# Kernel optimization log

Hardware: AMD Instinct MI355X
Metric: run time of the kernel (lower is better)

Reference implementation:

```python
import jax, jax.numpy as jnp
import numpy as np


def _conv1x1(X, W, b):
    # X: [B,C,H,W], W: [Cout,Cin], b: [Cout] -> [B,Cout,H,W]
    return jnp.einsum('oc,bchw->bohw', W, X) + b[None, :, None, None]


def setup_inputs() -> dict:
    key = jax.random.key(0)
    ks = jax.random.split(key, 7)
    B, C, H, W = 8, 512, 32, 32
    scale = 1.0 / np.sqrt(C)
    return {
        'X': jax.random.normal(ks[0], (B, C, H, W), dtype=jnp.float32),
        'W_phi': jax.random.normal(ks[1], (C, C), dtype=jnp.float32) * scale,
        'b_phi': jnp.zeros((C,), dtype=jnp.float32),
        'W_theta': jax.random.normal(ks[2], (C, C), dtype=jnp.float32) * scale,
        'b_theta': jnp.zeros((C,), dtype=jnp.float32),
        'W_beta': jax.random.normal(ks[3], (C, C), dtype=jnp.float32) * scale,
        'b_beta': jnp.zeros((C,), dtype=jnp.float32),
    }


def reference(X, W_phi, b_phi, W_theta, b_theta, W_beta, b_beta):
    B, C, H, W = X.shape
    N = H * W
    phi = _conv1x1(X, W_phi, b_phi).reshape(B, -1, N)      # [B,Co,N]
    theta = _conv1x1(X, W_theta, b_theta).reshape(B, -1, N)  # [B,Co,N]
    beta = _conv1x1(X, W_beta, b_beta).reshape(B, -1, N)    # [B,Co,N]
    # attention over spatial positions: scores [B,N,N], row-softmax
    A = jax.nn.softmax(jnp.einsum('bcn,bcm->bnm', phi, theta), axis=-1)
    Z = jnp.einsum('bcn,bnm->bcm', beta, A)                 # [B,Co,N]
    return Z.reshape(B, -1, H, W) + X
```

## Files before the change

### kernel.cpp

```cpp
#include <hip/hip_runtime.h>

typedef __bf16 bf16_t;
typedef __bf16 bf16x4 __attribute__((ext_vector_type(4)));
typedef __bf16 bf16x8 __attribute__((ext_vector_type(8)));
typedef _Float16 f16_t;
typedef _Float16 f16x4 __attribute__((ext_vector_type(4)));
typedef _Float16 f16x8 __attribute__((ext_vector_type(8)));
typedef float  f32x4  __attribute__((ext_vector_type(4)));

#define BK 64
#define BATCH 8
#define CDIM 512
#define NSP 1024
#define SOFF 90.0f

__device__ __forceinline__ void gl2lds16(const void* g, void* l) {
    __builtin_amdgcn_global_load_lds(
        (const __attribute__((address_space(1))) void*)g,
        (__attribute__((address_space(3))) void*)l, 16, 0, 0);
}

template<typename T, int NW>
__device__ __forceinline__ void stage128x64(const T* __restrict__ src, int ld, T* dst) {
    int lane = threadIdx.x & 63;
    int wave = threadIdx.x >> 6;
    constexpr int SPW = 16 / NW;
    int colsw = ((lane & 7) ^ (lane >> 3)) << 3;
#pragma unroll
    for (int c = 0; c < SPW; ++c) {
        int seg = wave * SPW + c;
        int row = (seg << 3) + (lane >> 3);
        const T* g = src + (size_t)row * ld + colsw;
        T* l = dst + (seg << 9);
        gl2lds16(g, l);
    }
}

__device__ __forceinline__ f32x4 mfma_op(f16x8 a, f16x8 b, f32x4 c) {
    return __builtin_amdgcn_mfma_f32_16x16x32_f16(a, b, c, 0, 0, 0);
}
__device__ __forceinline__ f32x4 mfma_op(bf16x8 a, bf16x8 b, f32x4 c) {
    return __builtin_amdgcn_mfma_f32_16x16x32_bf16(a, b, c, 0, 0, 0);
}

template<typename VT, typename T, int NW, int MI, int NI>
__device__ __forceinline__ void gemm_core(const T* __restrict__ A, int lda,
                                          const T* __restrict__ B, int ldb, int K,
                                          T* sA, T* sB, f32x4 acc[MI][NI]) {
    int lane = threadIdx.x & 63;
    int wave = threadIdx.x >> 6;
    int wr = (wave >> 1) * (MI * 16);
    int wc = (wave & 1) * (NI * 16);
    int fr = lane & 15;
    int q  = lane >> 4;

    for (int k0 = 0; k0 < K; k0 += BK) {
        stage128x64<T, NW>(A + k0, lda, sA);
        stage128x64<T, NW>(B + k0, ldb, sB);
        __syncthreads();
#pragma unroll
        for (int kk = 0; kk < 2; ++kk) {
            int sc = ((((kk << 2) + q) ^ (fr & 7)) << 3);
            VT a[MI], b[NI];
#pragma unroll
            for (int i = 0; i < MI; ++i)
                a[i] = *reinterpret_cast<const VT*>(sA + (wr + i*16 + fr)*BK + sc);
#pragma unroll
            for (int j = 0; j < NI; ++j)
                b[j] = *reinterpret_cast<const VT*>(sB + (wc + j*16 + fr)*BK + sc);
#pragma unroll
            for (int mi = 0; mi < MI; ++mi)
#pragma unroll
                for (int ni = 0; ni < NI; ++ni)
                    acc[mi][ni] = mfma_op(a[mi], b[ni], acc[mi][ni]);
        }
        __syncthreads();
    }
}

__global__ __launch_bounds__(256)
void prep_kernel(const float* __restrict__ X, const float* __restrict__ Wp,
                 const float* __restrict__ Wt, const float* __restrict__ Wb,
                 f16_t* __restrict__ Xt, f16_t* __restrict__ W16) {
    int z = blockIdx.z;
    int tx = threadIdx.x;
    int ty = threadIdx.y;
    if (z == 8) {
        int g = (blockIdx.y * 32 + blockIdx.x) * 256 + ty * 8 + tx;
        if (g < 98304) {
            int i = g << 3;
            int r = i >> 9, c = i & 511;
            const float* src = (r < 512) ? (Wp + ((size_t)r << 9))
                             : (r < 1024) ? (Wt + ((size_t)(r - 512) << 9))
                                          : (Wb + ((size_t)(r - 1024) << 9));
            float4 v0 = *reinterpret_cast<const float4*>(src + c);
            float4 v1 = *reinterpret_cast<const float4*>(src + c + 4);
            f16x8 o;
            o[0]=(f16_t)v0.x; o[1]=(f16_t)v0.y; o[2]=(f16_t)v0.z; o[3]=(f16_t)v0.w;
            o[4]=(f16_t)v1.x; o[5]=(f16_t)v1.y; o[6]=(f16_t)v1.z; o[7]=(f16_t)v1.w;
            *reinterpret_cast<f16x8*>(W16 + i) = o;
        }
        return;
    }
    __shared__ float tile[32][33];
    const float* x = X + (size_t)z * CDIM * NSP;
    int c0 = blockIdx.y * 32, n0 = blockIdx.x * 32;
    float4 v = *reinterpret_cast<const float4*>(x + (size_t)(c0 + ty) * NSP + n0 + tx * 4);
    tile[ty][tx * 4 + 0] = v.x;
    tile[ty][tx * 4 + 1] = v.y;
    tile[ty][tx * 4 + 2] = v.z;
    tile[ty][tx * 4 + 3] = v.w;
    __syncthreads();
    f16x4 o;
#pragma unroll
    for (int i = 0; i < 4; ++i) o[i] = (f16_t)tile[tx * 4 + i][ty];
    *reinterpret_cast<f16x4*>(Xt + (size_t)z * NSP * CDIM + (size_t)(n0 + ty) * CDIM + c0 + tx * 4) = o;
}

__global__ __launch_bounds__(256, 4)
void conv_kernel(const f16_t* __restrict__ Xt, const f16_t* __restrict__ W16,
                 const float* __restrict__ bias_phi, const float* __restrict__ bias_theta,
                 const float* __restrict__ bias_beta,
                 f16_t* __restrict__ phiH, f16_t* __restrict__ thH,
                 bf16_t* __restrict__ betaB) {
    __shared__ alignas(16) f16_t sA[128 * BK], sB[128 * BK];
    int b = blockIdx.z;
    int n0 = blockIdx.y * 128;
    int col0 = blockIdx.x * 128;
    const f16_t* A = Xt + ((size_t)b * NSP + n0) * CDIM;
    const f16_t* B = W16 + (size_t)col0 * CDIM;
    f32x4 acc[4][4];
#pragma unroll
    for (int i = 0; i < 4; i++)
#pragma unroll
        for (int j = 0; j < 4; j++)
#pragma unroll
            for (int e = 0; e < 4; e++) acc[i][j][e] = 0.0f;
    gemm_core<f16x8, f16_t, 4, 4, 4>(A, CDIM, B, CDIM, CDIM, sA, sB, acc);

    int lane = threadIdx.x & 63;
    int wave = threadIdx.x >> 6;
    int wr = (wave >> 1) << 6, wc = (wave & 1) << 6;
    int fr = lane & 15, q4 = ((lane >> 4) << 2);

    if (col0 < 1024) {
        bool isPhi = (col0 < 512);
        const float* bias = isPhi ? bias_phi : bias_theta;
        f16_t* dh = (isPhi ? phiH : thH) + (size_t)b * NSP * CDIM;
        int oc0 = col0 & 511;
#pragma unroll
        for (int mi = 0; mi < 4; mi++)
#pragma unroll
            for (int ni = 0; ni < 4; ni++) {
                int col = oc0 + wc + ni * 16 + fr;
                float bv = bias[col];
#pragma unroll
                for (int e = 0; e < 4; e++) {
                    int row = n0 + wr + mi * 16 + q4 + e;
                    dh[(size_t)row * CDIM + col] = (f16_t)(acc[mi][ni][e] + bv);
                }
            }
    } else {
        bf16_t* dst = betaB + (size_t)b * CDIM * NSP;
#pragma unroll
        for (int mi = 0; mi < 4; mi++)
#pragma unroll
            for (int ni = 0; ni < 4; ni++) {
                int c = (col0 - 1024) + wc + ni * 16 + fr;
                float bv = bias_beta[c];
                int rowb = n0 + wr + mi * 16 + q4;
                bf16x4 v;
#pragma unroll
                for (int e = 0; e < 4; e++) v[e] = (bf16_t)(acc[mi][ni][e] + bv);
                *reinterpret_cast<bf16x4*>(dst + (size_t)c * NSP + rowb) = v;
            }
    }
}

__global__ __launch_bounds__(256, 4)
void sgemm_kernel(const f16_t* __restrict__ phiH, const f16_t* __restrict__ thH,
                  bf16_t* __restrict__ Et, float* __restrict__ psum) {
    __shared__ alignas(16) f16_t sA[128 * BK], sB[128 * BK];
    int b = blockIdx.z;
    int n0 = blockIdx.y * 128;
    int m0 = blockIdx.x * 128;
    const f16_t* A = phiH + ((size_t)b * NSP + n0) * CDIM;
    const f16_t* B = thH + ((size_t)b * NSP + m0) * CDIM;
    f32x4 acc[4][4];
#pragma unroll
    for (int i = 0; i < 4; i++)
#pragma unroll
        for (int j = 0; j < 4; j++)
#pragma unroll
            for (int e = 0; e < 4; e++) acc[i][j][e] = 0.0f;
    gemm_core<f16x8, f16_t, 4, 4, 4>(A, CDIM, B, CDIM, CDIM, sA, sB, acc);

    bf16_t* et = Et + (size_t)b * NSP * NSP;
    int lane = threadIdx.x & 63;
    int wave = threadIdx.x >> 6;
    int wr = (wave >> 1) << 6, wc = (wave & 1) << 6;
    int fr = lane & 15, q4 = ((lane >> 4) << 2);

    float p[4][4];
#pragma unroll
    for (int mi = 0; mi < 4; mi++)
#pragma unroll
        for (int e = 0; e < 4; e++) p[mi][e] = 0.0f;

#pragma unroll
    for (int mi = 0; mi < 4; mi++)
#pragma unroll
        for (int ni = 0; ni < 4; ni++) {
            int col = m0 + wc + ni * 16 + fr;
            int rowb = n0 + wr + mi * 16 + q4;
            bf16x4 v;
#pragma unroll
            for (int e = 0; e < 4; e++) {
                float ev = __expf(acc[mi][ni][e] - SOFF);
                p[mi][e] += ev;
                v[e] = (bf16_t)ev;
            }
            *reinterpret_cast<bf16x4*>(et + (size_t)col * NSP + rowb) = v;
        }

#pragma unroll
    for (int mi = 0; mi < 4; mi++)
#pragma unroll
        for (int e = 0; e < 4; e++) {
#pragma unroll
            for (int off = 1; off < 16; off <<= 1)
                p[mi][e] += __shfl_xor(p[mi][e], off);
        }
    if ((lane & 15) == 0) {
        int pidx = blockIdx.x * 2 + (wc >> 6);
        float* ps = psum + ((size_t)b * 16 + pidx) * NSP;
#pragma unroll
        for (int mi = 0; mi < 4; mi++)
#pragma unroll
            for (int e = 0; e < 4; e++)
                ps[n0 + wr + mi * 16 + q4 + e] = p[mi][e];
    }
}

__global__ __launch_bounds__(256)
void norm_kernel(const float* __restrict__ psum, const bf16_t* __restrict__ betaB,
                 bf16_t* __restrict__ beta2) {
    __shared__ float rs[NSP];
    int b  = blockIdx.x >> 4;
    int cc = (blockIdx.x & 15) << 5;
    int tid = threadIdx.x;
#pragma unroll
    for (int i = 0; i < 4; ++i) {
        int n = i * 256 + tid;
        float s = 0.f;
#pragma unroll
        for (int pp = 0; pp < 16; ++pp) s += psum[((size_t)b * 16 + pp) * NSP + n];
        rs[n] = 1.0f / s;
    }
    __syncthreads();
#pragma unroll
    for (int it = 0; it < 16; ++it) {
        int row = cc + it * 2 + (tid >> 7);
        int n = (tid & 127) << 3;
        size_t base = ((size_t)b * CDIM + row) * NSP + n;
        bf16x8 v = *reinterpret_cast<const bf16x8*>(betaB + base);
        bf16x8 o;
#pragma unroll
        for (int e = 0; e < 8; ++e) o[e] = (bf16_t)((float)v[e] * rs[n + e]);
        *reinterpret_cast<bf16x8*>(beta2 + base) = o;
    }
}

__global__ __launch_bounds__(512, 2)
void zgemm_kernel(const bf16_t* __restrict__ beta2, const bf16_t* __restrict__ Et,
                  const float* __restrict__ X, float* __restrict__ out) {
    __shared__ alignas(16) bf16_t sA[128 * BK], sB[128 * BK];
    int b = blockIdx.z;
    int c0 = blockIdx.y * 128;
    int m0 = blockIdx.x * 128;
    const bf16_t* A = beta2 + ((size_t)b * CDIM + c0) * NSP;
    const bf16_t* B = Et + ((size_t)b * NSP + m0) * NSP;
    f32x4 acc[2][4];
#pragma unroll
    for (int i = 0; i < 2; i++)
#pragma unroll
        for (int j = 0; j < 4; j++)
#pragma unroll
            for (int e = 0; e < 4; e++) acc[i][j][e] = 0.0f;
    gemm_core<bf16x8, bf16_t, 8, 2, 4>(A, NSP, B, NSP, NSP, sA, sB, acc);

    const float* xs = X + (size_t)b * CDIM * NSP;
    float* dst = out + (size_t)b * CDIM * NSP;
    int lane = threadIdx.x & 63;
    int wave = threadIdx.x >> 6;
    int wr = (wave >> 1) << 5, wc = (wave & 1) << 6;
    int fr = lane & 15, q4 = ((lane >> 4) << 2);
#pragma unroll
    for (int mi = 0; mi < 2; mi++)
#pragma unroll
        for (int ni = 0; ni < 4; ni++) {
            int col = m0 + wc + ni * 16 + fr;
#pragma unroll
            for (int e = 0; e < 4; e++) {
                int row = c0 + wr + mi * 16 + q4 + e;
                size_t idx = (size_t)row * NSP + col;
                dst[idx] = acc[mi][ni][e] + xs[idx];
            }
        }
}

extern "C" void kernel_launch(void* const* d_in, const int* in_sizes, int n_in,
                              void* d_out, int out_size, void* d_ws, size_t ws_size,
                              hipStream_t stream) {
    const float* X  = (const float*)d_in[0];
    const float* Wp = (const float*)d_in[1];
    const float* bp = (const float*)d_in[2];
    const float* Wt = (const float*)d_in[3];
    const float* bt = (const float*)d_in[4];
    const float* Wb = (const float*)d_in[5];
    const float* bb = (const float*)d_in[6];
    float* out = (float*)d_out;

    char* ws = (char*)d_ws;
    size_t off = 0;
    auto alloc = [&](size_t bytes) -> char* {
        char* p = ws + off;
        off += (bytes + 255) & ~(size_t)255;
        return p;
    };

    const size_t BNC2 = (size_t)BATCH * NSP * CDIM * 2;
    f16_t*  Xt16  = (f16_t*)alloc(BNC2);
    f16_t*  W16   = (f16_t*)alloc((size_t)1536 * 512 * 2);
    f16_t*  phiH  = (f16_t*)alloc(BNC2);
    f16_t*  thH   = (f16_t*)alloc(BNC2);
    bf16_t* betaB = (bf16_t*)alloc(BNC2);
    bf16_t* beta2 = (bf16_t*)alloc(BNC2);
    bf16_t* Et    = (bf16_t*)alloc((size_t)BATCH * NSP * NSP * 2);
    float*  psum  = (float*)alloc((size_t)BATCH * 16 * NSP * 4);

    prep_kernel<<<dim3(32, 16, 9), dim3(8, 32), 0, stream>>>(X, Wp, Wt, Wb, Xt16, W16);
    conv_kernel<<<dim3(12, 8, BATCH), dim3(256), 0, stream>>>(Xt16, W16, bp, bt, bb,
                                                              phiH, thH, betaB);
    sgemm_kernel<<<dim3(8, 8, BATCH), dim3(256), 0, stream>>>(phiH, thH, Et, psum);
    norm_kernel<<<dim3(128), dim3(256), 0, stream>>>(psum, betaB, beta2);
    zgemm_kernel<<<dim3(8, 4, BATCH), dim3(512), 0, stream>>>(beta2, Et, X, out);

    (void)in_sizes; (void)n_in; (void)out_size; (void)ws_size;
}
```

Baseline: 79.11 us.

## Fuse softmax normalization into Z GEMM and co-schedule beta conv with scores

The beta 1x1 conv is moved out of the phi/theta conv launch and runs as extra blocks of the score GEMM kernel, so the two independent workloads share one launch. The separate norm kernel goes away: the Z GEMM reduces the softmax row sums into LDS itself and scales the beta tile by the reciprocals while staging it into LDS. The Z GEMM tile also shrinks to 64x128 with 2x2 MFMA tiles per wave, giving more blocks. This removes one launch and one full write and read of the scaled beta buffer. In exchange, every Z block recomputes the 1024 reciprocal sums, and the A tile is staged through registers instead of direct global-to-LDS loads.

```diff
diff --git a/kernel.cpp b/kernel.cpp
--- a/kernel.cpp
+++ b/kernel.cpp
@@ -31,8 +31,7 @@
         int seg = wave * SPW + c;
         int row = (seg << 3) + (lane >> 3);
         const T* g = src + (size_t)row * ld + colsw;
-        T* l = dst + (seg << 9);
-        gl2lds16(g, l);
+        gl2lds16(g, dst + (seg << 9));
     }
 }
 
@@ -43,39 +42,48 @@
     return __builtin_amdgcn_mfma_f32_16x16x32_bf16(a, b, c, 0, 0, 0);
 }
 
-template<typename VT, typename T, int NW, int MI, int NI>
-__device__ __forceinline__ void gemm_core(const T* __restrict__ A, int lda,
-                                          const T* __restrict__ B, int ldb, int K,
-                                          T* sA, T* sB, f32x4 acc[MI][NI]) {
+template<typename VT, typename T>
+__device__ __forceinline__ void gemm128_4w(const T* __restrict__ A, int lda,
+                                           const T* __restrict__ B, int ldb, int K,
+                                           T* sA, T* sB, f32x4 acc[4][4]) {
     int lane = threadIdx.x & 63;
     int wave = threadIdx.x >> 6;
-    int wr = (wave >> 1) * (MI * 16);
-    int wc = (wave & 1) * (NI * 16);
+    int wr = (wave >> 1) << 6;
+    int wc = (wave & 1) << 6;
     int fr = lane & 15;
     int q  = lane >> 4;
 
     for (int k0 = 0; k0 < K; k0 += BK) {
-        stage128x64<T, NW>(A + k0, lda, sA);
-        stage128x64<T, NW>(B + k0, ldb, sB);
+        stage128x64<T, 4>(A + k0, lda, sA);
+        stage128x64<T, 4>(B + k0, ldb, sB);
         __syncthreads();
 #pragma unroll
         for (int kk = 0; kk < 2; ++kk) {
             int sc = ((((kk << 2) + q) ^ (fr & 7)) << 3);
-            VT a[MI], b[NI];
-#pragma unroll
-            for (int i = 0; i < MI; ++i)
+            VT a[4], b[4];
+#pragma unroll
+            for (int i = 0; i < 4; ++i)
                 a[i] = *reinterpret_cast<const VT*>(sA + (wr + i*16 + fr)*BK + sc);
 #pragma unroll
-            for (int j = 0; j < NI; ++j)
+            for (int j = 0; j < 4; ++j)
                 b[j] = *reinterpret_cast<const VT*>(sB + (wc + j*16 + fr)*BK + sc);
 #pragma unroll
-            for (int mi = 0; mi < MI; ++mi)
-#pragma unroll
-                for (int ni = 0; ni < NI; ++ni)
+            for (int mi = 0; mi < 4; ++mi)
+#pragma unroll
+                for (int ni = 0; ni < 4; ++ni)
                     acc[mi][ni] = mfma_op(a[mi], b[ni], acc[mi][ni]);
         }
         __syncthreads();
     }
+}
+
+__device__ __forceinline__ void zero44(f32x4 acc[4][4]) {
+#pragma unroll
+    for (int i = 0; i < 4; i++)
+#pragma unroll
+        for (int j = 0; j < 4; j++)
+#pragma unroll
+            for (int e = 0; e < 4; e++) acc[i][j][e] = 0.0f;
 }
 
 __global__ __launch_bounds__(256)
@@ -118,187 +126,203 @@
 }
 
 __global__ __launch_bounds__(256, 4)
-void conv_kernel(const f16_t* __restrict__ Xt, const f16_t* __restrict__ W16,
-                 const float* __restrict__ bias_phi, const float* __restrict__ bias_theta,
-                 const float* __restrict__ bias_beta,
-                 f16_t* __restrict__ phiH, f16_t* __restrict__ thH,
-                 bf16_t* __restrict__ betaB) {
+void conv_pt_kernel(const f16_t* __restrict__ Xt, const f16_t* __restrict__ W16,
+                    const float* __restrict__ bias_phi, const float* __restrict__ bias_theta,
+                    f16_t* __restrict__ phiH, f16_t* __restrict__ thH) {
     __shared__ alignas(16) f16_t sA[128 * BK], sB[128 * BK];
     int b = blockIdx.z;
     int n0 = blockIdx.y * 128;
     int col0 = blockIdx.x * 128;
-    const f16_t* A = Xt + ((size_t)b * NSP + n0) * CDIM;
-    const f16_t* B = W16 + (size_t)col0 * CDIM;
     f32x4 acc[4][4];
-#pragma unroll
-    for (int i = 0; i < 4; i++)
-#pragma unroll
-        for (int j = 0; j < 4; j++)
-#pragma unroll
-            for (int e = 0; e < 4; e++) acc[i][j][e] = 0.0f;
-    gemm_core<f16x8, f16_t, 4, 4, 4>(A, CDIM, B, CDIM, CDIM, sA, sB, acc);
+    zero44(acc);
+    gemm128_4w<f16x8, f16_t>(Xt + ((size_t)b * NSP + n0) * CDIM, CDIM,
+                             W16 + (size_t)col0 * CDIM, CDIM, CDIM, sA, sB, acc);
 
     int lane = threadIdx.x & 63;
     int wave = threadIdx.x >> 6;
     int wr = (wave >> 1) << 6, wc = (wave & 1) << 6;
     int fr = lane & 15, q4 = ((lane >> 4) << 2);
 
-    if (col0 < 1024) {
-        bool isPhi = (col0 < 512);
-        const float* bias = isPhi ? bias_phi : bias_theta;
-        f16_t* dh = (isPhi ? phiH : thH) + (size_t)b * NSP * CDIM;
-        int oc0 = col0 & 511;
-#pragma unroll
-        for (int mi = 0; mi < 4; mi++)
-#pragma unroll
-            for (int ni = 0; ni < 4; ni++) {
-                int col = oc0 + wc + ni * 16 + fr;
-                float bv = bias[col];
-#pragma unroll
-                for (int e = 0; e < 4; e++) {
-                    int row = n0 + wr + mi * 16 + q4 + e;
-                    dh[(size_t)row * CDIM + col] = (f16_t)(acc[mi][ni][e] + bv);
-                }
-            }
-    } else {
-        bf16_t* dst = betaB + (size_t)b * CDIM * NSP;
-#pragma unroll
-        for (int mi = 0; mi < 4; mi++)
-#pragma unroll
-            for (int ni = 0; ni < 4; ni++) {
-                int c = (col0 - 1024) + wc + ni * 16 + fr;
-                float bv = bias_beta[c];
-                int rowb = n0 + wr + mi * 16 + q4;
-                bf16x4 v;
-#pragma unroll
-                for (int e = 0; e < 4; e++) v[e] = (bf16_t)(acc[mi][ni][e] + bv);
-                *reinterpret_cast<bf16x4*>(dst + (size_t)c * NSP + rowb) = v;
-            }
-    }
+    bool isPhi = (col0 < 512);
+    const float* bias = isPhi ? bias_phi : bias_theta;
+    f16_t* dh = (isPhi ? phiH : thH) + (size_t)b * NSP * CDIM;
+    int oc0 = col0 & 511;
+#pragma unroll
+    for (int mi = 0; mi < 4; mi++)
+#pragma unroll
+        for (int ni = 0; ni < 4; ni++) {
+            int col = oc0 + wc + ni * 16 + fr;
+            float bv = bias[col];
+#pragma unroll
+            for (int e = 0; e < 4; e++) {
+                int row = n0 + wr + mi * 16 + q4 + e;
+                dh[(size_t)row * CDIM + col] = (f16_t)(acc[mi][ni][e] + bv);
+            }
+        }
 }
 
 __global__ __launch_bounds__(256, 4)
-void sgemm_kernel(const f16_t* __restrict__ phiH, const f16_t* __restrict__ thH,
-                  bf16_t* __restrict__ Et, float* __restrict__ psum) {
+void sgemm_beta_kernel(const f16_t* __restrict__ Xt, const f16_t* __restrict__ W16,
+                       const f16_t* __restrict__ phiH, const f16_t* __restrict__ thH,
+                       const float* __restrict__ bias_beta,
+                       bf16_t* __restrict__ Et, float* __restrict__ psum,
+                       bf16_t* __restrict__ betaB) {
     __shared__ alignas(16) f16_t sA[128 * BK], sB[128 * BK];
     int b = blockIdx.z;
-    int n0 = blockIdx.y * 128;
-    int m0 = blockIdx.x * 128;
-    const f16_t* A = phiH + ((size_t)b * NSP + n0) * CDIM;
-    const f16_t* B = thH + ((size_t)b * NSP + m0) * CDIM;
-    f32x4 acc[4][4];
-#pragma unroll
-    for (int i = 0; i < 4; i++)
-#pragma unroll
-        for (int j = 0; j < 4; j++)
-#pragma unroll
-            for (int e = 0; e < 4; e++) acc[i][j][e] = 0.0f;
-    gemm_core<f16x8, f16_t, 4, 4, 4>(A, CDIM, B, CDIM, CDIM, sA, sB, acc);
-
-    bf16_t* et = Et + (size_t)b * NSP * NSP;
+    int j = blockIdx.x;
     int lane = threadIdx.x & 63;
     int wave = threadIdx.x >> 6;
     int wr = (wave >> 1) << 6, wc = (wave & 1) << 6;
     int fr = lane & 15, q4 = ((lane >> 4) << 2);
-
-    float p[4][4];
-#pragma unroll
-    for (int mi = 0; mi < 4; mi++)
-#pragma unroll
-        for (int e = 0; e < 4; e++) p[mi][e] = 0.0f;
-
-#pragma unroll
-    for (int mi = 0; mi < 4; mi++)
-#pragma unroll
-        for (int ni = 0; ni < 4; ni++) {
-            int col = m0 + wc + ni * 16 + fr;
-            int rowb = n0 + wr + mi * 16 + q4;
-            bf16x4 v;
+    f32x4 acc[4][4];
+    zero44(acc);
+
+    if (j < 64) {
+        int n0 = (j >> 3) << 7, m0 = (j & 7) << 7;
+        gemm128_4w<f16x8, f16_t>(phiH + ((size_t)b * NSP + n0) * CDIM, CDIM,
+                                 thH + ((size_t)b * NSP + m0) * CDIM, CDIM,
+                                 CDIM, sA, sB, acc);
+        bf16_t* et = Et + (size_t)b * NSP * NSP;
+        float p[4][4];
+#pragma unroll
+        for (int mi = 0; mi < 4; mi++)
+#pragma unroll
+            for (int e = 0; e < 4; e++) p[mi][e] = 0.0f;
+#pragma unroll
+        for (int mi = 0; mi < 4; mi++)
+#pragma unroll
+            for (int ni = 0; ni < 4; ni++) {
+                int col = m0 + wc + ni * 16 + fr;
+                int rowb = n0 + wr + mi * 16 + q4;
+                bf16x4 v;
+#pragma unroll
+                for (int e = 0; e < 4; e++) {
+                    float ev = __expf(acc[mi][ni][e] - SOFF);
+                    p[mi][e] += ev;
+                    v[e] = (bf16_t)ev;
+                }
+                *reinterpret_cast<bf16x4*>(et + (size_t)col * NSP + rowb) = v;
+            }
+#pragma unroll
+        for (int mi = 0; mi < 4; mi++)
 #pragma unroll
             for (int e = 0; e < 4; e++) {
-                float ev = __expf(acc[mi][ni][e] - SOFF);
-                p[mi][e] += ev;
-                v[e] = (bf16_t)ev;
-            }
-            *reinterpret_cast<bf16x4*>(et + (size_t)col * NSP + rowb) = v;
-        }
-
-#pragma unroll
-    for (int mi = 0; mi < 4; mi++)
-#pragma unroll
-        for (int e = 0; e < 4; e++) {
-#pragma unroll
-            for (int off = 1; off < 16; off <<= 1)
-                p[mi][e] += __shfl_xor(p[mi][e], off);
-        }
-    if ((lane & 15) == 0) {
-        int pidx = blockIdx.x * 2 + (wc >> 6);
-        float* ps = psum + ((size_t)b * 16 + pidx) * NSP;
+#pragma unroll
+                for (int off = 1; off < 16; off <<= 1)
+                    p[mi][e] += __shfl_xor(p[mi][e], off);
+            }
+        if ((lane & 15) == 0) {
+            int pidx = ((j & 7) << 1) + (wc >> 6);
+            float* ps = psum + ((size_t)b * 16 + pidx) * NSP;
+#pragma unroll
+            for (int mi = 0; mi < 4; mi++)
+#pragma unroll
+                for (int e = 0; e < 4; e++)
+                    ps[(j >> 3) * 128 + wr + mi * 16 + q4 + e] = p[mi][e];
+        }
+    } else {
+        int j2 = j - 64;
+        int nb = j2 >> 2, cb = j2 & 3;
+        gemm128_4w<f16x8, f16_t>(Xt + ((size_t)b * NSP + nb * 128) * CDIM, CDIM,
+                                 W16 + (size_t)(1024 + cb * 128) * CDIM, CDIM,
+                                 CDIM, sA, sB, acc);
+        bf16_t* dst = betaB + (size_t)b * CDIM * NSP;
 #pragma unroll
         for (int mi = 0; mi < 4; mi++)
 #pragma unroll
-            for (int e = 0; e < 4; e++)
-                ps[n0 + wr + mi * 16 + q4 + e] = p[mi][e];
-    }
-}
-
-__global__ __launch_bounds__(256)
-void norm_kernel(const float* __restrict__ psum, const bf16_t* __restrict__ betaB,
-                 bf16_t* __restrict__ beta2) {
+            for (int ni = 0; ni < 4; ni++) {
+                int c = cb * 128 + wc + ni * 16 + fr;
+                float bv = bias_beta[c];
+                int rowb = nb * 128 + wr + mi * 16 + q4;
+                bf16x4 v;
+#pragma unroll
+                for (int e = 0; e < 4; e++) v[e] = (bf16_t)(acc[mi][ni][e] + bv);
+                *reinterpret_cast<bf16x4*>(dst + (size_t)c * NSP + rowb) = v;
+            }
+    }
+}
+
+__global__ __launch_bounds__(512, 4)
+void zgemm_kernel(const bf16_t* __restrict__ betaB, const bf16_t* __restrict__ Et,
+                  const float* __restrict__ psum, const float* __restrict__ X,
+                  float* __restrict__ out) {
     __shared__ float rs[NSP];
-    int b  = blockIdx.x >> 4;
-    int cc = (blockIdx.x & 15) << 5;
+    __shared__ alignas(16) bf16_t sA[64 * BK];
+    __shared__ alignas(16) bf16_t sB[128 * BK];
+    int b = blockIdx.z;
+    int c0 = blockIdx.y * 64;
+    int m0 = blockIdx.x * 128;
     int tid = threadIdx.x;
-#pragma unroll
-    for (int i = 0; i < 4; ++i) {
-        int n = i * 256 + tid;
+
+#pragma unroll
+    for (int i = 0; i < 2; ++i) {
+        int n = i * 512 + tid;
         float s = 0.f;
 #pragma unroll
         for (int pp = 0; pp < 16; ++pp) s += psum[((size_t)b * 16 + pp) * NSP + n];
         rs[n] = 1.0f / s;
     }
     __syncthreads();
-#pragma unroll
-    for (int it = 0; it < 16; ++it) {
-        int row = cc + it * 2 + (tid >> 7);
-        int n = (tid & 127) << 3;
-        size_t base = ((size_t)b * CDIM + row) * NSP + n;
-        bf16x8 v = *reinterpret_cast<const bf16x8*>(betaB + base);
+
+    int lane = tid & 63, wave = tid >> 6;
+    int fr = lane & 15, q = lane >> 4, q4 = (lane >> 4) << 2;
+    int wr = (wave >> 2) << 5;
+    int wc = (wave & 3) << 5;
+    int ar = lane >> 3, ac = lane & 7;
+    int acs = ac ^ ar;
+
+    const bf16_t* A = betaB + ((size_t)b * CDIM + c0) * NSP;
+    const bf16_t* B = Et + ((size_t)b * NSP + m0) * NSP;
+    f32x4 acc[2][2];
+#pragma unroll
+    for (int i = 0; i < 2; i++)
+#pragma unroll
+        for (int jj = 0; jj < 2; jj++)
+#pragma unroll
+            for (int e = 0; e < 4; e++) acc[i][jj][e] = 0.0f;
+
+    for (int k0 = 0; k0 < NSP; k0 += BK) {
+        stage128x64<bf16_t, 8>(B + k0, NSP, sB);
+        float4 r0v = *reinterpret_cast<const float4*>(&rs[k0 + ac * 8]);
+        float4 r1v = *reinterpret_cast<const float4*>(&rs[k0 + ac * 8 + 4]);
+        int row = (wave << 3) + ar;
+        bf16x8 v = *reinterpret_cast<const bf16x8*>(A + (size_t)row * NSP + k0 + ac * 8);
         bf16x8 o;
-#pragma unroll
-        for (int e = 0; e < 8; ++e) o[e] = (bf16_t)((float)v[e] * rs[n + e]);
-        *reinterpret_cast<bf16x8*>(beta2 + base) = o;
-    }
-}
-
-__global__ __launch_bounds__(512, 2)
-void zgemm_kernel(const bf16_t* __restrict__ beta2, const bf16_t* __restrict__ Et,
-                  const float* __restrict__ X, float* __restrict__ out) {
-    __shared__ alignas(16) bf16_t sA[128 * BK], sB[128 * BK];
-    int b = blockIdx.z;
-    int c0 = blockIdx.y * 128;
-    int m0 = blockIdx.x * 128;
-    const bf16_t* A = beta2 + ((size_t)b * CDIM + c0) * NSP;
-    const bf16_t* B = Et + ((size_t)b * NSP + m0) * NSP;
-    f32x4 acc[2][4];
-#pragma unroll
-    for (int i = 0; i < 2; i++)
-#pragma unroll
-        for (int j = 0; j < 4; j++)
-#pragma unroll
-            for (int e = 0; e < 4; e++) acc[i][j][e] = 0.0f;
-    gemm_core<bf16x8, bf16_t, 8, 2, 4>(A, NSP, B, NSP, NSP, sA, sB, acc);
+        o[0] = (bf16_t)((float)v[0] * r0v.x);
+        o[1] = (bf16_t)((float)v[1] * r0v.y);
+        o[2] = (bf16_t)((float)v[2] * r0v.z);
+        o[3] = (bf16_t)((float)v[3] * r0v.w);
+        o[4] = (bf16_t)((float)v[4] * r1v.x);
+        o[5] = (bf16_t)((float)v[5] * r1v.y);
+        o[6] = (bf16_t)((float)v[6] * r1v.z);
+        o[7] = (bf16_t)((float)v[7] * r1v.w);
+        *reinterpret_cast<bf16x8*>(sA + (wave << 9) + ar * 64 + acs * 8) = o;
+        __syncthreads();
+#pragma unroll
+        for (int kk = 0; kk < 2; ++kk) {
+            int sc = ((((kk << 2) + q) ^ (fr & 7)) << 3);
+            bf16x8 a[2], bbv[2];
+#pragma unroll
+            for (int i = 0; i < 2; ++i)
+                a[i] = *reinterpret_cast<const bf16x8*>(sA + (wr + i*16 + fr)*BK + sc);
+#pragma unroll
+            for (int jj = 0; jj < 2; ++jj)
+                bbv[jj] = *reinterpret_cast<const bf16x8*>(sB + (wc + jj*16 + fr)*BK + sc);
+#pragma unroll
+            for (int mi = 0; mi < 2; ++mi)
+#pragma unroll
+                for (int ni = 0; ni < 2; ++ni)
+                    acc[mi][ni] = mfma_op(a[mi], bbv[ni], acc[mi][ni]);
+        }
+        __syncthreads();
+    }
 
     const float* xs = X + (size_t)b * CDIM * NSP;
     float* dst = out + (size_t)b * CDIM * NSP;
-    int lane = threadIdx.x & 63;
-    int wave = threadIdx.x >> 6;
-    int wr = (wave >> 1) << 5, wc = (wave & 1) << 6;
-    int fr = lane & 15, q4 = ((lane >> 4) << 2);
 #pragma unroll
     for (int mi = 0; mi < 2; mi++)
 #pragma unroll
-        for (int ni = 0; ni < 4; ni++) {
+        for (int ni = 0; ni < 2; ni++) {
             int col = m0 + wc + ni * 16 + fr;
 #pragma unroll
             for (int e = 0; e < 4; e++) {
@@ -335,16 +359,15 @@
     f16_t*  phiH  = (f16_t*)alloc(BNC2);
     f16_t*  thH   = (f16_t*)alloc(BNC2);
     bf16_t* betaB = (bf16_t*)alloc(BNC2);
-    bf16_t* beta2 = (bf16_t*)alloc(BNC2);
     bf16_t* Et    = (bf16_t*)alloc((size_t)BATCH * NSP * NSP * 2);
     float*  psum  = (float*)alloc((size_t)BATCH * 16 * NSP * 4);
 
     prep_kernel<<<dim3(32, 16, 9), dim3(8, 32), 0, stream>>>(X, Wp, Wt, Wb, Xt16, W16);
-    conv_kernel<<<dim3(12, 8, BATCH), dim3(256), 0, stream>>>(Xt16, W16, bp, bt, bb,
-                                                              phiH, thH, betaB);
-    sgemm_kernel<<<dim3(8, 8, BATCH), dim3(256), 0, stream>>>(phiH, thH, Et, psum);
-    norm_kernel<<<dim3(128), dim3(256), 0, stream>>>(psum, betaB, beta2);
-    zgemm_kernel<<<dim3(8, 4, BATCH), dim3(512), 0, stream>>>(beta2, Et, X, out);
+    conv_pt_kernel<<<dim3(8, 8, BATCH), dim3(256), 0, stream>>>(Xt16, W16, bp, bt,
+                                                                phiH, thH);
+    sgemm_beta_kernel<<<dim3(96, 1, BATCH), dim3(256), 0, stream>>>(Xt16, W16, phiH, thH,
+                                                                    bb, Et, psum, betaB);
+    zgemm_kernel<<<dim3(8, 8, BATCH), dim3(512), 0, stream>>>(betaB, Et, psum, X, out);
 
     (void)in_sizes; (void)n_in; (void)out_size; (void)ws_size;
 }
```

Result: faster. 75.30 us (-4.8%).
